# Kernel optimization log

Measured on AMD Instinct MI355X. Metric: run time of the kernel, lower is better.

## Reference

```python
import jax, jax.numpy as jnp
import numpy as np

HEADS = 9
MODEL_DIM = 256
LN_EPS = 1e-5


def _relative_features(h, w):
    # grid[i, j] = (i, j); rel[i, j, k, l] = (k - i, l - j)
    r = jnp.arange(h if h >= w else w)
    gi, gj = jnp.meshgrid(jnp.arange(h), jnp.arange(w), indexing='ij')
    grid = jnp.stack([gi, gj], axis=-1).astype(jnp.float32)          # (h, w, 2)
    rel = grid[None, None, :, :, :] - grid[:, :, None, None, :]       # (h, w, h, w, 2)
    cross = (rel[..., 0] * rel[..., 1])[..., None]
    return jnp.concatenate([rel, rel ** 2, cross], axis=-1)           # (h, w, h, w, 5)


def _layer_norm(x, gamma, beta):
    mu = jnp.mean(x, axis=-1, keepdims=True)
    var = jnp.var(x, axis=-1, keepdims=True)
    return (x - mu) * jax.lax.rsqrt(var + LN_EPS) * gamma + beta


def setup_inputs() -> dict:
    key = jax.random.key(0)
    ks = jax.random.split(key, 6)
    bs, h, w = 16, 32, 32
    hidden_state = jax.random.normal(ks[0], (bs, h, w, MODEL_DIM), dtype=jnp.float32)
    attention_centers = 2.0 * jax.random.normal(ks[1], (HEADS, 2), dtype=jnp.float32)
    attention_spreads = jnp.eye(2, dtype=jnp.float32)[None] + 0.01 * jax.random.normal(
        ks[2], (HEADS, 2, 2), dtype=jnp.float32)
    # torch Linear(in=heads*model_dim, out=model_dim): weight (out, in)
    fan_in = HEADS * MODEL_DIM
    bound = 1.0 / np.sqrt(fan_in)
    value_w = jax.random.uniform(ks[3], (MODEL_DIM, fan_in), jnp.float32, -bound, bound)
    value_b = jax.random.uniform(ks[4], (MODEL_DIM,), jnp.float32, -bound, bound)
    ln_gamma = jnp.ones((MODEL_DIM,), jnp.float32)
    ln_beta = jnp.zeros((MODEL_DIM,), jnp.float32)
    return {
        'hidden_state': hidden_state,
        'attention_centers': attention_centers,
        'attention_spreads': attention_spreads,
        'value_w': value_w,
        'value_b': value_b,
        'ln_gamma': ln_gamma,
        'ln_beta': ln_beta,
    }


def reference(hidden_state, attention_centers, attention_spreads, value_w, value_b,
              ln_gamma, ln_beta):
    bs, h, w, d = hidden_state.shape
    # pre_norm=True: normalize first, residual uses normalized hidden (as in source)
    x = _layer_norm(hidden_state, ln_gamma, ln_beta)

    # per-head quadratic target vector u (faithful to source, incl. the (c + mu_2) term)
    inv_cov = jnp.einsum('hij,hkj->hik', attention_spreads, attention_spreads)
    a, b, c = inv_cov[:, 0, 0], inv_cov[:, 0, 1], inv_cov[:, 1, 1]
    mu1, mu2 = attention_centers[:, 0], attention_centers[:, 1]
    u = -0.5 * jnp.stack(
        [-2 * (a * mu1 + b * mu2), -2 * (c + mu2 + b * mu1), a, c, 2 * b], axis=-1)  # (H, 5)

    R = _relative_features(h, w)                                      # (h, w, h, w, 5)
    scores = jnp.einsum('ijkld,hd->ijhkl', R, u)                      # (h, w, H, h, w)
    probs = jax.nn.softmax(scores.reshape(h, w, HEADS, h * w), axis=-1)
    probs = probs.reshape(h, w, HEADS, h, w)
    # dropout prob = 0 (eval mode)

    context = jnp.einsum('ijhkl,bkld->bijhd', probs, x)               # (bs, h, w, H, d)
    context = context.reshape(bs, h, w, HEADS * d)
    output = context @ value_w.T + value_b
    output = output + x
    return output, probs
```

## Files before the change

### kernel.cpp

```cpp
#include <hip/hip_runtime.h>
#include <hip/hip_bf16.h>
#include <stdint.h>

typedef __bf16 bf16;
typedef __bf16 bf16x4 __attribute__((ext_vector_type(4)));
typedef __bf16 bf16x8 __attribute__((ext_vector_type(8)));
typedef float  f32x4  __attribute__((ext_vector_type(4)));

#define GLDS16(g, l) __builtin_amdgcn_global_load_lds(                      \
    (const __attribute__((address_space(1))) void*)(g),                     \
    (__attribute__((address_space(3))) void*)(l), 16, 0, 0)

#define BARX() do { __builtin_amdgcn_s_barrier();                            \
                    __builtin_amdgcn_sched_barrier(0); } while (0)
#define VMW(n) do { asm volatile("s_waitcnt vmcnt(" #n ")" ::: "memory");    \
                    __builtin_amdgcn_sched_barrier(0); } while (0)

#define TRUNC_S 14.0f

__global__ __launch_bounds__(256) void k_lnt(const float* __restrict__ hs,
                                             const float* __restrict__ gamma,
                                             const float* __restrict__ beta,
                                             bf16* __restrict__ xb,
                                             bf16* __restrict__ xt) {
  __shared__ bf16 tile[4][32][66];
  int kl0 = blockIdx.x * 32, b = blockIdx.y;
  int t = threadIdx.x, lane = t & 63, w = t >> 6;
  float4 g  = ((const float4*)gamma)[lane];
  float4 be = ((const float4*)beta)[lane];
  int sq = lane >> 4, col = (lane & 15) * 4;
#pragma unroll
  for (int i = 0; i < 8; i++) {
    int r = w * 8 + i;
    size_t row = (size_t)b * 1024 + kl0 + r;
    float4 v = ((const float4*)(hs + row * 256))[lane];
    float s  = v.x + v.y + v.z + v.w;
    float s2 = v.x*v.x + v.y*v.y + v.z*v.z + v.w*v.w;
#pragma unroll
    for (int o = 32; o; o >>= 1) { s += __shfl_xor(s, o); s2 += __shfl_xor(s2, o); }
    float mu = s * (1.0f/256.0f);
    float var = s2 * (1.0f/256.0f) - mu*mu;
    float rs = rsqrtf(var + 1e-5f);
    bf16x4 o4;
    o4[0] = (bf16)((v.x - mu) * rs * g.x + be.x);
    o4[1] = (bf16)((v.y - mu) * rs * g.y + be.y);
    o4[2] = (bf16)((v.z - mu) * rs * g.z + be.z);
    o4[3] = (bf16)((v.w - mu) * rs * g.w + be.w);
    *(bf16x4*)(xb + row * 256 + lane * 4) = o4;
    *(bf16x4*)(&tile[sq][r][col]) = o4;
  }
  __syncthreads();
  int dr = t >> 2, k0 = (t & 3) * 8;
#pragma unroll
  for (int q = 0; q < 4; q++) {
    bf16x8 w0;
#pragma unroll
    for (int i = 0; i < 8; i++) w0[i] = tile[q][k0 + i][dr];
    *(bf16x8*)(xt + ((size_t)(b * 256 + q * 64 + dr)) * 1024 + kl0 + k0) = w0;
  }
}

__global__ __launch_bounds__(256) void k_vwb(const float* __restrict__ vw,
                                             bf16* __restrict__ vwb,
                                             const float* __restrict__ centers,
                                             const float* __restrict__ spreads,
                                             int* __restrict__ sorted) {
  __shared__ int nt[72];
  int t = threadIdx.x;
  if (blockIdx.x == 288) {
    if (t < 72) {
      int h = t >> 3, mb = t & 7;
      float S00 = spreads[h*4+0], S01 = spreads[h*4+1];
      float S10 = spreads[h*4+2], S11 = spreads[h*4+3];
      float a_ = S00*S00 + S01*S01;
      float b_ = S00*S10 + S01*S11;
      float c_ = S10*S10 + S11*S11;
      float mu1 = centers[h*2+0], mu2 = centers[h*2+1];
      float det = fmaxf(a_*c_ - b_*b_, 1e-6f);
      float A_ = a_*mu1 + b_*mu2;
      float B_ = c_ + mu2 + b_*mu1;
      float ustar = (c_*A_ - b_*B_) / det;
      float lam = fmaxf(a_ - b_*b_/c_, 1e-3f);
      float M_ = __fsqrt_rn(TRUNC_S / lam) + 1.5f;
      float lo_f = (float)(mb*4) + ustar, hi_f = lo_f + 3.0f;
      int k_lo = (int)floorf(fminf(lo_f, 31.0f) - M_);
      int k_hi = (int)ceilf(fmaxf(hi_f, 0.0f) + M_) + 1;
      if (k_lo < 0) k_lo = 0;
      if (k_hi > 32) k_hi = 32;
      if (k_hi <= k_lo) { k_lo = 0; k_hi = 32; }
      nt[t] = k_hi - k_lo;
    }
    __syncthreads();
    if (t < 72) {
      int my = nt[t], r = 0;
#pragma unroll 1
      for (int j = 0; j < 72; j++) {
        int v = nt[j];
        if (v > my || (v == my && j < t)) r++;
      }
      sorted[r] = t;
    }
    return;
  }
  int i = (blockIdx.x * 256 + t) * 8;
  float4 q0 = *(const float4*)(vw + i);
  float4 q1 = *(const float4*)(vw + i + 4);
  bf16x8 o;
  o[0]=(bf16)q0.x; o[1]=(bf16)q0.y; o[2]=(bf16)q0.z; o[3]=(bf16)q0.w;
  o[4]=(bf16)q1.x; o[5]=(bf16)q1.y; o[6]=(bf16)q1.z; o[7]=(bf16)q1.w;
  *(bf16x8*)(vwb + i) = o;
}

__global__ __launch_bounds__(256) void k_probs(const float* __restrict__ centers,
                                               const float* __restrict__ spreads,
                                               float* __restrict__ pf,
                                               bf16* __restrict__ pb2) {
  int bid = blockIdx.x;
  int h  = bid % 9;
  int ij = bid / 9;
  int i = ij >> 5, j = ij & 31;
  float S00 = spreads[h*4+0], S01 = spreads[h*4+1];
  float S10 = spreads[h*4+2], S11 = spreads[h*4+3];
  float a  = S00*S00 + S01*S01;
  float bq = S00*S10 + S01*S11;
  float c  = S10*S10 + S11*S11;
  float mu1 = centers[h*2+0], mu2 = centers[h*2+1];
  float u0 = a*mu1 + bq*mu2;
  float u1 = c + mu2 + bq*mu1;
  float u2 = -0.5f*a, u3 = -0.5f*c, u4 = -bq;
  int t = threadIdx.x;
  float sc[4]; float mx = -1e30f;
#pragma unroll
  for (int s = 0; s < 4; s++) {
    int kl = t*4 + s;
    float d0 = (float)((kl >> 5) - i);
    float d1 = (float)((kl & 31) - j);
    float v = d0*(u0 + u2*d0) + d1*(u1 + u3*d1) + u4*d0*d1;
    sc[s] = v; mx = fmaxf(mx, v);
  }
  __shared__ float red[8];
#pragma unroll
  for (int o = 32; o; o >>= 1) mx = fmaxf(mx, __shfl_xor(mx, o));
  int lane = t & 63, wid = t >> 6;
  if (lane == 0) red[wid] = mx;
  __syncthreads();
  mx = fmaxf(fmaxf(red[0], red[1]), fmaxf(red[2], red[3]));
  float sum = 0.f;
#pragma unroll
  for (int s = 0; s < 4; s++) { sc[s] = __expf(sc[s] - mx); sum += sc[s]; }
#pragma unroll
  for (int o = 32; o; o >>= 1) sum += __shfl_xor(sum, o);
  if (lane == 0) red[4 + wid] = sum;
  __syncthreads();
  sum = red[4] + red[5] + red[6] + red[7];
  float inv = 1.0f / sum;
  float4 o;
  o.x = sc[0]*inv; o.y = sc[1]*inv; o.z = sc[2]*inv; o.w = sc[3]*inv;
  *(float4*)(pf + (size_t)bid*1024 + t*4) = o;
  bf16x4 ob;
  ob[0] = (bf16)o.x; ob[1] = (bf16)o.y; ob[2] = (bf16)o.z; ob[3] = (bf16)o.w;
  *(bf16x4*)(pb2 + ((size_t)(h*32 + (t >> 3))*1024 + ij)*32 + (t & 7)*4) = ob;
}

__device__ __forceinline__ bf16x8 frag_ld(const bf16* base, int row, int g) {
  return *(const bf16x8*)(base + row*32 + ((g ^ ((row >> 1) & 3)) << 3));
}

__global__ __launch_bounds__(256, 2) void k_ctx(const bf16* __restrict__ pb2,
                                                const bf16* __restrict__ xt,
                                                const float* __restrict__ centers,
                                                const float* __restrict__ spreads,
                                                const int* __restrict__ sorted,
                                                bf16* __restrict__ ctx,
                                                int b0, int nbt) {
  __shared__ bf16 Bs[3*8192];
  int r_  = blockIdx.x / nbt;
  int nb  = blockIdx.x % nbt;
  int cls = sorted[r_];
  int h   = cls >> 3;
  int mb  = cls & 7;
  int ij0 = mb * 128;
  int nrow0 = (b0 + nb) * 256;

  int t = threadIdx.x, lane = t & 63, w = t >> 6;
  int wr = w >> 1, wc = w & 1;
  int g = lane >> 4, rl = lane & 15;

  float S00 = spreads[h*4+0], S01 = spreads[h*4+1];
  float S10 = spreads[h*4+2], S11 = spreads[h*4+3];
  float a_ = S00*S00 + S01*S01;
  float b_ = S00*S10 + S01*S11;
  float c_ = S10*S10 + S11*S11;
  float mu1 = centers[h*2+0], mu2 = centers[h*2+1];
  float det = fmaxf(a_*c_ - b_*b_, 1e-6f);
  float A_ = a_*mu1 + b_*mu2;
  float B_ = c_ + mu2 + b_*mu1;
  float ustar = (c_*A_ - b_*B_) / det;
  float lam = fmaxf(a_ - b_*b_/c_, 1e-3f);
  float M_ = __fsqrt_rn(TRUNC_S / lam) + 1.5f;
  float lo_f = (float)(mb*4) + ustar, hi_f = lo_f + 3.0f;
  int k_lo = (int)floorf(fminf(lo_f, 31.0f) - M_);
  int k_hi = (int)ceilf(fmaxf(hi_f, 0.0f) + M_) + 1;
  if (k_lo < 0) k_lo = 0;
  if (k_hi > 32) k_hi = 32;
  if (k_hi <= k_lo) { k_lo = 0; k_hi = 32; }
  const int NT = k_hi - k_lo;

  f32x4 acc[4][8];
#pragma unroll
  for (int x_ = 0; x_ < 4; x_++)
#pragma unroll
    for (int y_ = 0; y_ < 8; y_++) acc[x_][y_] = (f32x4){0.f,0.f,0.f,0.f};

  int arow = t >> 2;
  int acs  = (t & 3) ^ ((t >> 3) & 3);
  const bf16* b1 = xt + (size_t)(nrow0 + arow) * 1024 + k_lo*32 + acs * 8;
  const bf16* aP = pb2 + ((size_t)(h*32 + k_lo)*1024 + ij0 + wr*64 + rl)*32 + g*8;

#define STG(sb, kt) do {                                                    \
    _Pragma("unroll")                                                       \
    for (int q = 0; q < 4; q++)                                             \
      GLDS16(b1 + (size_t)q*64*1024 + (kt)*32,                              \
             ((char*)Bs) + (sb)*16384 + q*4096 + t*16);                     \
  } while (0)

#define LOADA(AF, kt) do {                                                  \
    const bf16* a_p = aP + (size_t)(kt)*32768;                              \
    _Pragma("unroll")                                                       \
    for (int fr = 0; fr < 4; fr++)                                          \
      AF[fr] = *(const bf16x8*)(a_p + fr*512);                              \
  } while (0)

#define MFM(AF, BF) do {                                                    \
    _Pragma("unroll")                                                       \
    for (int fr = 0; fr < 4; fr++)                                          \
      _Pragma("unroll")                                                     \
      for (int fn = 0; fn < 8; fn++)                                        \
        acc[fr][fn] = __builtin_amdgcn_mfma_f32_16x16x32_bf16(              \
            AF[fr], BF[fn], acc[fr][fn], 0, 0, 0);                          \
  } while (0)

  bf16x8 afA[4], afB[4];
  STG(0, 0);
  if (NT > 1) STG(1, 1);
  __builtin_amdgcn_sched_barrier(0);
  LOADA(afA, 0);
  if (NT > 1) VMW(8); else VMW(4);
  BARX();

  int cur = 0, kt = 0;
  while (true) {
    {
      bf16x8 bf_[8];
#pragma unroll
      for (int fn = 0; fn < 8; fn++) bf_[fn] = frag_ld(Bs + cur*8192, wc*128 + fn*16 + rl, g);
      int sb = cur + 2; if (sb >= 3) sb -= 3;
      if (kt + 2 < NT) STG(sb, kt + 2);
      __builtin_amdgcn_sched_barrier(0);
      if (kt + 1 < NT) LOADA(afB, kt + 1);
      MFM(afA, bf_);
      if (kt + 1 >= NT) break;
      if (kt + 2 < NT) VMW(8); else VMW(4);
      BARX();
      cur = cur + 1; if (cur >= 3) cur = 0;
      kt++;
    }
    {
      bf16x8 bf_[8];
#pragma unroll
      for (int fn = 0; fn < 8; fn++) bf_[fn] = frag_ld(Bs + cur*8192, wc*128 + fn*16 + rl, g);
      int sb = cur + 2; if (sb >= 3) sb -= 3;
      if (kt + 2 < NT) STG(sb, kt + 2);
      __builtin_amdgcn_sched_barrier(0);
      if (kt + 1 < NT) LOADA(afA, kt + 1);
      MFM(afB, bf_);
      if (kt + 1 >= NT) break;
      if (kt + 2 < NT) VMW(8); else VMW(4);
      BARX();
      cur = cur + 1; if (cur >= 3) cur = 0;
      kt++;
    }
  }
#undef STG
#undef LOADA
#undef MFM

#pragma unroll
  for (int fr = 0; fr < 4; fr++) {
    int row = ij0 + wr*64 + fr*16 + g*4;
#pragma unroll
    for (int fn = 0; fn < 8; fn++) {
      int d = wc*128 + fn*16 + rl;
      size_t base = ((size_t)nb*1024 + row) * 2304 + h*256 + d;
      f32x4 a4 = acc[fr][fn];
#pragma unroll
      for (int r = 0; r < 4; r++)
        ctx[base + (size_t)r*2304] = (bf16)a4[r];
    }
  }
}

__global__ __launch_bounds__(512, 1) void k_out(const bf16* __restrict__ ctx,
                                                const bf16* __restrict__ vwb,
                                                const bf16* __restrict__ xb,
                                                const float* __restrict__ vbias,
                                                float* __restrict__ out, int b0) {
  __shared__ bf16 lds[3 * 20480];
  int t = threadIdx.x, lane = t & 63, w = t >> 6;
  int wr = w >> 2, wc = w & 3;
  int g = lane >> 4, rl = lane & 15;
  int r0 = blockIdx.x * 64;
  char* ldsb = (char*)lds;

  f32x4 acc[2][4];
#pragma unroll
  for (int x_ = 0; x_ < 2; x_++)
#pragma unroll
    for (int y_ = 0; y_ < 4; y_++) acc[x_][y_] = (f32x4){0.f,0.f,0.f,0.f};

  int rr  = t >> 3;
  int csw = (t & 7) ^ (rr & 7);
  const bf16* aS = ctx + (size_t)(r0 + rr) * 2304 + csw * 8;
  const bf16* bS = vwb + (size_t)rr * 2304 + csw * 8;

#define STGO(sb, kt) do {                                                     \
    GLDS16(aS + (kt)*64, ldsb + (sb)*40960 + t*16);                           \
    _Pragma("unroll")                                                         \
    for (int q = 0; q < 4; q++)                                               \
      GLDS16(bS + (size_t)q*64*2304 + (kt)*64,                                \
             ldsb + (sb)*40960 + 8192 + q*8192 + t*16);                       \
  } while (0)

  STGO(0, 0); STGO(1, 1);
  VMW(5);
  BARX();

  int cur = 0;
  for (int kt = 0; kt < 36; ++kt) {
    int sb = cur + 2; if (sb >= 3) sb -= 3;
    const char* ab = ldsb + cur*40960;
    const char* bb = ab + 8192;
    bf16x8 af0[2], af1[2], bf0[4], bf1[4];
#pragma unroll
    for (int fr = 0; fr < 2; fr++) {
      int row_ = wr*32 + fr*16 + rl;
      af0[fr] = *(const bf16x8*)(ab + row_*128 + (((g  ) ^ (row_&7)) << 4));
      af1[fr] = *(const bf16x8*)(ab + row_*128 + (((g+4) ^ (row_&7)) << 4));
    }
#pragma unroll
    for (int fn = 0; fn < 4; fn++) {
      int row_ = wc*64 + fn*16 + rl;
      bf0[fn] = *(const bf16x8*)(bb + row_*128 + (((g  ) ^ (row_&7)) << 4));
      bf1[fn] = *(const bf16x8*)(bb + row_*128 + (((g+4) ^ (row_&7)) << 4));
    }
    if (kt + 2 < 36) STGO(sb, kt + 2);
    BARX();
    __builtin_amdgcn_s_setprio(1);
#pragma unroll
    for (int fr = 0; fr < 2; fr++)
#pragma unroll
      for (int fn = 0; fn < 4; fn++) {
        acc[fr][fn] = __builtin_amdgcn_mfma_f32_16x16x32_bf16(af0[fr], bf0[fn], acc[fr][fn], 0, 0, 0);
        acc[fr][fn] = __builtin_amdgcn_mfma_f32_16x16x32_bf16(af1[fr], bf1[fn], acc[fr][fn], 0, 0, 0);
      }
    __builtin_amdgcn_s_setprio(0);
    if (kt + 2 < 36)      VMW(5);
    else if (kt + 1 < 36) VMW(0);
    BARX();
    cur = cur + 1; if (cur >= 3) cur = 0;
  }
#undef STGO

#pragma unroll
  for (int fr = 0; fr < 2; fr++) {
    int rowl = r0 + wr*32 + fr*16 + g*4;
    size_t rowg = (size_t)b0*1024 + rowl;
#pragma unroll
    for (int fn = 0; fn < 4; fn++) {
      int m = wc*64 + fn*16 + rl;
      float bv = vbias[m];
      size_t base = rowg*256 + m;
#pragma unroll
      for (int r = 0; r < 4; r++)
        out[base + (size_t)r*256] = acc[fr][fn][r] + bv + (float)xb[base + (size_t)r*256];
    }
  }
}

extern "C" void kernel_launch(void* const* d_in, const int* in_sizes, int n_in,
                              void* d_out, int out_size, void* d_ws, size_t ws_size,
                              hipStream_t stream) {
  const float* hs      = (const float*)d_in[0];
  const float* centers = (const float*)d_in[1];
  const float* spreads = (const float*)d_in[2];
  const float* vw      = (const float*)d_in[3];
  const float* vb      = (const float*)d_in[4];
  const float* gamma   = (const float*)d_in[5];
  const float* beta    = (const float*)d_in[6];
  float* out     = (float*)d_out;
  float* probs_f = out + 4194304;

  char* ws = (char*)d_ws;
  bf16* xb  = (bf16*)ws;
  bf16* pb2 = (bf16*)(ws + 8388608);
  bf16* xt  = (bf16*)(ws + 27262976);
  bf16* vwb = (bf16*)(ws + 35651584);
  bf16* ctx = (bf16*)(ws + 36831232);

  int CB = 16;
  while (CB > 1 && 36831232ull + (size_t)CB * 4718592ull + 512ull > ws_size) CB >>= 1;
  int* sortedp = (int*)(ws + 36831232 + (size_t)CB * 4718592ull);

  k_lnt<<<dim3(32, 16), 256, 0, stream>>>(hs, gamma, beta, xb, xt);
  k_probs<<<9216, 256, 0, stream>>>(centers, spreads, probs_f, pb2);
  k_vwb<<<289, 256, 0, stream>>>(vw, vwb, centers, spreads, sortedp);
  for (int b0 = 0; b0 < 16; b0 += CB) {
    int c = (16 - b0) < CB ? (16 - b0) : CB;
    k_ctx<<<dim3(72 * c), 256, 0, stream>>>(pb2, xt, centers, spreads, sortedp, ctx, b0, c);
    k_out<<<dim3(c*16), 512, 0, stream>>>(ctx, vwb, xb, vb, out, b0);
  }
}
```

Baseline: 103.3 us.

## Skip bf16 prob writes outside truncated window; vectorize ctx stores via swapped MFMA operands

The softmax kernel now computes a per-head, per-row-block window of key rows where the Gaussian-like probabilities are non-negligible. It writes the bf16 copy of the probabilities only inside that window, cutting global write traffic. Separately, the MFMA operands in the context kernel are swapped so each lane holds four consecutive d values, letting the epilogue write one 8-byte bf16x4 store instead of four strided 2-byte stores. The skipped bf16 entries are left stale or uninitialized unless the consumer also restricts its K range. This relies on truncation assumptions about the score shape.

After: 117.3 us. +13.6%, slower.

```diff
diff --git a/kernel.cpp b/kernel.cpp
--- a/kernel.cpp
+++ b/kernel.cpp
@@ -157,9 +157,28 @@
   float4 o;
   o.x = sc[0]*inv; o.y = sc[1]*inv; o.z = sc[2]*inv; o.w = sc[3]*inv;
   *(float4*)(pf + (size_t)bid*1024 + t*4) = o;
-  bf16x4 ob;
-  ob[0] = (bf16)o.x; ob[1] = (bf16)o.y; ob[2] = (bf16)o.z; ob[3] = (bf16)o.w;
-  *(bf16x4*)(pb2 + ((size_t)(h*32 + (t >> 3))*1024 + ij)*32 + (t & 7)*4) = ob;
+  {
+    int mb = i >> 2;
+    float a_ = a, b_ = bq, c_ = c;
+    float det = fmaxf(a_*c_ - b_*b_, 1e-6f);
+    float A_ = a_*mu1 + b_*mu2;
+    float B_ = c_ + mu2 + b_*mu1;
+    float ustar = (c_*A_ - b_*B_) / det;
+    float lam = fmaxf(a_ - b_*b_/c_, 1e-3f);
+    float M_ = __fsqrt_rn(TRUNC_S / lam) + 1.5f;
+    float lo_f = (float)(mb*4) + ustar, hi_f = lo_f + 3.0f;
+    int k_lo = (int)floorf(fminf(lo_f, 31.0f) - M_);
+    int k_hi = (int)ceilf(fmaxf(hi_f, 0.0f) + M_) + 1;
+    if (k_lo < 0) k_lo = 0;
+    if (k_hi > 32) k_hi = 32;
+    if (k_hi <= k_lo) { k_lo = 0; k_hi = 32; }
+    int ktc = t >> 3;
+    if (ktc >= k_lo && ktc < k_hi) {
+      bf16x4 ob;
+      ob[0] = (bf16)o.x; ob[1] = (bf16)o.y; ob[2] = (bf16)o.z; ob[3] = (bf16)o.w;
+      *(bf16x4*)(pb2 + ((size_t)(h*32 + ktc)*1024 + ij)*32 + (t & 7)*4) = ob;
+    }
+  }
 }
 
 __device__ __forceinline__ bf16x8 frag_ld(const bf16* base, int row, int g) {
@@ -237,7 +256,7 @@
       _Pragma("unroll")                                                     \
       for (int fn = 0; fn < 8; fn++)                                        \
         acc[fr][fn] = __builtin_amdgcn_mfma_f32_16x16x32_bf16(              \
-            AF[fr], BF[fn], acc[fr][fn], 0, 0, 0);                          \
+            BF[fn], AF[fr], acc[fr][fn], 0, 0, 0);                          \
   } while (0)
 
   bf16x8 afA[4], afB[4];
@@ -287,15 +306,16 @@
 
 #pragma unroll
   for (int fr = 0; fr < 4; fr++) {
-    int row = ij0 + wr*64 + fr*16 + g*4;
+    int ij = ij0 + wr*64 + fr*16 + rl;
+    size_t rowbase = ((size_t)nb*1024 + ij) * 2304 + h*256;
 #pragma unroll
     for (int fn = 0; fn < 8; fn++) {
-      int d = wc*128 + fn*16 + rl;
-      size_t base = ((size_t)nb*1024 + row) * 2304 + h*256 + d;
+      int d0 = wc*128 + fn*16 + g*4;
       f32x4 a4 = acc[fr][fn];
-#pragma unroll
-      for (int r = 0; r < 4; r++)
-        ctx[base + (size_t)r*2304] = (bf16)a4[r];
+      bf16x4 o4;
+      o4[0] = (bf16)a4[0]; o4[1] = (bf16)a4[1];
+      o4[2] = (bf16)a4[2]; o4[3] = (bf16)a4[3];
+      *(bf16x4*)(ctx + rowbase + d0) = o4;
     }
   }
 }
```
